# Performance work log

Hardware: AMD Instinct MI355X
Metric: run time of the kernel (lower is better)

The kernel has to match this reference:

```python
import jax, jax.numpy as jnp
import numpy as np

B = 16384      # batch
FEAT = 4096    # features
D = 64         # nearest_root_factors(4096) -> (64, 64)
BN_EPS = 1e-3


def setup_inputs() -> dict:
    key = jax.random.key(0)
    ks = jax.random.split(key, 9)
    stdv1 = 1.0 / np.sqrt(D)   # layer1: zero_initialization=False path
    stdv2 = 0.001              # layer2: zero_initialization=True path

    def u(k, shape, s):
        return jax.random.uniform(k, shape, minval=-s, maxval=s, dtype=jnp.float32)

    return {
        "inputs": jax.random.normal(ks[0], (B, FEAT), dtype=jnp.float32),
        "bn0_gamma": jnp.ones((FEAT,), jnp.float32),
        "bn0_beta": jnp.zeros((FEAT,), jnp.float32),
        "bn1_gamma": jnp.ones((FEAT,), jnp.float32),
        "bn1_beta": jnp.zeros((FEAT,), jnp.float32),
        # Kronecker layer 1 (left: weights (o2=input_dim1, o1=out_dim1); right: (d,d))
        "k1_lw": u(ks[1], (D, D), stdv1),
        "k1_lb": u(ks[2], (D, D), stdv1),
        "k1_rw": u(ks[3], (D, D), stdv1),
        "k1_rb": u(ks[4], (D, D), stdv1),
        # Kronecker layer 2 (zero-initialized)
        "k2_lw": u(ks[5], (D, D), stdv2),
        "k2_lb": u(ks[6], (D, D), stdv2),
        "k2_rw": u(ks[7], (D, D), stdv2),
        "k2_rb": u(ks[8], (D, D), stdv2),
    }


def _batch_norm(x, gamma, beta):
    # training-mode BN: biased batch statistics over the batch dim, eps=1e-3
    m = jnp.mean(x, axis=0)
    v = jnp.var(x, axis=0)
    return (x - m) * jax.lax.rsqrt(v + BN_EPS) * gamma + beta


def _kron_block(t, lw, lb, rw, rb):
    # KDLeftLayer: permute(matmul(permute(x,[0,2,1]), W),[0,2,1]) + b
    #   out[b,o,j] = sum_k x[b,k,j] * W[k,o]
    t = jnp.einsum("bkj,ko->boj", t, lw) + lb
    # KDRightLayer: x @ W + b
    t = jnp.matmul(t, rw) + rb
    return t


def reference(inputs, bn0_gamma, bn0_beta, bn1_gamma, bn1_beta,
              k1_lw, k1_lb, k1_rw, k1_rb, k2_lw, k2_lb, k2_rw, k2_rb):
    t = jax.nn.relu(_batch_norm(inputs, bn0_gamma, bn0_beta))
    t = t.reshape(-1, D, D)
    t = _kron_block(t, k1_lw, k1_lb, k1_rw, k1_rb).reshape(-1, FEAT)
    t = jax.nn.relu(_batch_norm(t, bn1_gamma, bn1_beta))
    # dropout p=0.0 -> identity
    t = t.reshape(-1, D, D)
    t = _kron_block(t, k2_lw, k2_lb, k2_rw, k2_rb).reshape(-1, FEAT)
    return inputs + t
```

## Files before the change

kernel.cpp:

```cpp
#include <hip/hip_runtime.h>

#define NROWS 16384
#define NFEAT 4096

typedef __attribute__((ext_vector_type(8))) short          bfrag8;
typedef __attribute__((ext_vector_type(4))) float          fvec4;
typedef __attribute__((ext_vector_type(2))) float          fvec2;
typedef __attribute__((ext_vector_type(4))) unsigned short usvec4;
typedef __attribute__((ext_vector_type(8))) unsigned short usvec8;
typedef __attribute__((ext_vector_type(2))) unsigned int   uvec2;

#define WS_P0   ((size_t)0)
#define WS_P1   ((size_t)16 << 20)
#define WS_SC0  ((size_t)48 << 20)
#define WS_SH0  (WS_SC0 + 16384)
#define WS_SC1  (WS_SC0 + 32768)
#define WS_SH1  (WS_SC0 + 49152)
#define WS_C1   (WS_SC0 + 65536)
#define WS_C2   (WS_SC0 + 81920)
#define WS_T1   ((size_t)64 << 20)
#define WS_XB   ((size_t)192 << 20)

__device__ __forceinline__ unsigned short f2bf_bits(float f) {
  unsigned u = __builtin_bit_cast(unsigned, f);
  u += 0x7FFFu + ((u >> 16) & 1u);
  return (unsigned short)(u >> 16);
}
__device__ __forceinline__ float bf2f(unsigned short b) {
  return __builtin_bit_cast(float, ((unsigned)b) << 16);
}
__device__ __forceinline__ usvec4 pack4(fvec4 a) {
  usvec4 p;
#pragma unroll
  for (int e = 0; e < 4; ++e) p[e] = f2bf_bits(a[e]);
  return p;
}
__device__ __forceinline__ fvec4 unpack4(usvec4 p) {
  return fvec4{bf2f(p[0]), bf2f(p[1]), bf2f(p[2]), bf2f(p[3])};
}

__global__ __launch_bounds__(256) void k_bn0part(const float* __restrict__ x,
                                                 unsigned short* __restrict__ p0,
                                                 unsigned short* __restrict__ xb) {
  const int t = threadIdx.x, p = blockIdx.x;
  fvec4 s[4], sq[4];
#pragma unroll
  for (int q = 0; q < 4; ++q) { s[q] = fvec4{0.f,0.f,0.f,0.f}; sq[q] = s[q]; }
  for (int r = p * 16; r < p * 16 + 16; ++r) {
    const fvec4* row = (const fvec4*)(x + (size_t)r * NFEAT);
    usvec4* xrow = (usvec4*)(xb + (size_t)r * NFEAT);
#pragma unroll
    for (int q = 0; q < 4; ++q) {
      fvec4 v = row[t + 256 * q];
      s[q] += v; sq[q] += v * v;
      xrow[t + 256 * q] = pack4(v);
    }
  }
#pragma unroll
  for (int q = 0; q < 4; ++q) {
    int f0 = (t + 256 * q) * 4;
    *(usvec4*)(p0 + (size_t)p * 8192 + f0)        = pack4(s[q]);
    *(usvec4*)(p0 + (size_t)p * 8192 + 4096 + f0) = pack4(sq[q]);
  }
}

__device__ __forceinline__ void red_body(fvec4 (*red)[16][2],
                                         const unsigned short* __restrict__ parts,
                                         int nsets,
                                         const float* __restrict__ g,
                                         const float* __restrict__ bta,
                                         float* __restrict__ sc_out,
                                         float* __restrict__ sh_out, int j) {
  const int t = threadIdx.x;
  const int fc = t & 15, c = t >> 4;
  const int v = j * 64 + fc * 4;
  fvec4 s = fvec4{0.f,0.f,0.f,0.f}, q = s;
  for (int i = c; i < nsets; i += 16) {
    s += unpack4(*(const usvec4*)(parts + (size_t)i * 8192 + v));
    q += unpack4(*(const usvec4*)(parts + (size_t)i * 8192 + 4096 + v));
  }
  red[c][fc][0] = s; red[c][fc][1] = q;
  __syncthreads();
  if (c == 0) {
    fvec4 S = red[0][fc][0], Q = red[0][fc][1];
#pragma unroll
    for (int k = 1; k < 16; ++k) { S += red[k][fc][0]; Q += red[k][fc][1]; }
    fvec4 SC, SH;
    const float inv = 1.0f / NROWS;
#pragma unroll
    for (int e = 0; e < 4; ++e) {
      float mean = S[e] * inv;
      float var  = Q[e] * inv - mean * mean;
      float scv  = g[v + e] * rsqrtf(var + 1e-3f);
      SC[e] = scv; SH[e] = bta[v + e] - mean * scv;
    }
    *(fvec4*)(sc_out + v) = SC;
    *(fvec4*)(sh_out + v) = SH;
  }
}

__global__ __launch_bounds__(256) void k_prep0(const unsigned short* __restrict__ p0,
                                               const float* __restrict__ g0,
                                               const float* __restrict__ b0,
                                               float* __restrict__ sc0,
                                               float* __restrict__ sh0,
                                               const float* __restrict__ lb1,
                                               const float* __restrict__ rw1,
                                               const float* __restrict__ rb1,
                                               const float* __restrict__ lb2,
                                               const float* __restrict__ rw2,
                                               const float* __restrict__ rb2,
                                               float* __restrict__ c1,
                                               float* __restrict__ c2) {
  __shared__ fvec4 red[16][16][2];
  if (blockIdx.x < 64) {
    red_body(red, p0, 1024, g0, b0, sc0, sh0, blockIdx.x);
  } else {
    const int bb   = blockIdx.x - 64;
    const int idx  = (bb & 15) * 256 + threadIdx.x;
    const int part = bb >> 4;
    const float* lb = part ? lb2 : lb1;
    const float* rw = part ? rw2 : rw1;
    const float* rb = part ? rb2 : rb1;
    int r = idx >> 6, o = idx & 63;
    float acc = rb[o * 64 + r];
    for (int j = 0; j < 64; ++j) acc += lb[o * 64 + j] * rw[j * 64 + r];
    (part ? c2 : c1)[o * 64 + r] = acc;
  }
}

__global__ __launch_bounds__(256) void k_red1(const unsigned short* __restrict__ p1,
                                              const float* __restrict__ g1,
                                              const float* __restrict__ b1,
                                              float* __restrict__ sc1,
                                              float* __restrict__ sh1) {
  __shared__ fvec4 red[16][16][2];
  red_body(red, p1, 2048, g1, b1, sc1, sh1, blockIdx.x);
}

template <int LAYER, int RPBN>
__global__ __launch_bounds__(256) void k_kron(const unsigned short* __restrict__ xb,
                                              const float* __restrict__ lw,
                                              const float* __restrict__ rw,
                                              const float* __restrict__ scv,
                                              const float* __restrict__ shv,
                                              const float* __restrict__ cn,
                                              unsigned char* __restrict__ t1q,
                                              float* __restrict__ outf,
                                              unsigned short* __restrict__ p1) {
  __shared__ unsigned short vt[2][64 * 64];
  const int tid = threadIdx.x, bid = blockIdx.x;
  const int w = tid >> 6, l = tid & 63, m = l & 15, g = l >> 4;
  const int r0 = bid * RPBN;

  bfrag8 frw[4][2];
#pragma unroll
  for (int rt = 0; rt < 4; ++rt)
#pragma unroll
    for (int ks = 0; ks < 2; ++ks)
#pragma unroll
      for (int i = 0; i < 8; ++i)
        frw[rt][ks][i] = (short)f2bf_bits(rw[(ks * 32 + g * 8 + i) * 64 + rt * 16 + m]);

  bfrag8 flw[2];
#pragma unroll
  for (int ks = 0; ks < 2; ++ks)
#pragma unroll
    for (int i = 0; i < 8; ++i)
      flw[ks][i] = (short)f2bf_bits(lw[(ks * 32 + g * 8 + i) * 64 + w * 16 + m]);

  fvec4 cb[4];
#pragma unroll
  for (int rt = 0; rt < 4; ++rt)
    cb[rt] = *(const fvec4*)(cn + (w * 16 + m) * 64 + rt * 16 + g * 4);

  float sc[2][8], sh[2][8];
#pragma unroll
  for (int ks = 0; ks < 2; ++ks) {
    int f = (w * 16 + m) * 64 + ks * 32 + g * 8;
    fvec4 a0 = *(const fvec4*)(scv + f), a1 = *(const fvec4*)(scv + f + 4);
    fvec4 h0 = *(const fvec4*)(shv + f), h1 = *(const fvec4*)(shv + f + 4);
#pragma unroll
    for (int e = 0; e < 4; ++e) {
      sc[ks][e] = a0[e]; sc[ks][4 + e] = a1[e];
      sh[ks][e] = h0[e]; sh[ks][4 + e] = h1[e];
    }
  }

  fvec4 s1[4], q1[4];
#pragma unroll
  for (int rt = 0; rt < 4; ++rt) { s1[rt] = fvec4{0.f,0.f,0.f,0.f}; q1[rt] = s1[rt]; }

  usvec8 pfa[2][2];
  uvec2  pfq[2][2];
  usvec4 pfr[2][4];

  if constexpr (LAYER == 1) {
    const usvec8* pt0 = (const usvec8*)(xb + (size_t)r0 * NFEAT);
    const usvec8* pt1 = (const usvec8*)(xb + (size_t)(r0 + 1) * NFEAT);
    pfa[0][0] = pt0[(w * 16 + m) * 8 + g];
    pfa[0][1] = pt0[(w * 16 + m) * 8 + 4 + g];
    pfa[1][0] = pt1[(w * 16 + m) * 8 + g];
    pfa[1][1] = pt1[(w * 16 + m) * 8 + 4 + g];
  } else {
    const uvec2* pq0 = (const uvec2*)(t1q + (size_t)r0 * NFEAT);
    const uvec2* pq1 = (const uvec2*)(t1q + (size_t)(r0 + 1) * NFEAT);
    pfq[0][0] = pq0[(w * 16 + m) * 8 + g];
    pfq[0][1] = pq0[(w * 16 + m) * 8 + 4 + g];
    pfq[1][0] = pq1[(w * 16 + m) * 8 + g];
    pfq[1][1] = pq1[(w * 16 + m) * 8 + 4 + g];
#pragma unroll
    for (int rt = 0; rt < 4; ++rt) {
      int off = (w * 16 + m) * 64 + rt * 16 + g * 4;
      pfr[0][rt] = *(const usvec4*)(xb + (size_t)r0 * NFEAT + off);
      pfr[1][rt] = *(const usvec4*)(xb + (size_t)(r0 + 1) * NFEAT + off);
    }
  }

#pragma unroll
  for (int rr = 0; rr < RPBN; ++rr) {
    const int b = r0 + rr;
    const int cur = rr & 1;

    bfrag8 fa[2];
    if constexpr (LAYER == 1) {
#pragma unroll
      for (int ks = 0; ks < 2; ++ks) {
        usvec8 tv = pfa[cur][ks];
#pragma unroll
        for (int i = 0; i < 8; ++i) {
          float y = fmaxf(bf2f(tv[i]) * sc[ks][i] + sh[ks][i], 0.f);
          fa[ks][i] = (short)f2bf_bits(y);
        }
      }
    } else {
#pragma unroll
      for (int ks = 0; ks < 2; ++ks) {
        uvec2 tv = pfq[cur][ks];
        fvec2 d0 = __builtin_amdgcn_cvt_pk_f32_fp8((int)tv[0], false);
        fvec2 d1 = __builtin_amdgcn_cvt_pk_f32_fp8((int)tv[0], true);
        fvec2 d2 = __builtin_amdgcn_cvt_pk_f32_fp8((int)tv[1], false);
        fvec2 d3 = __builtin_amdgcn_cvt_pk_f32_fp8((int)tv[1], true);
        float xv[8] = {d0[0], d0[1], d1[0], d1[1], d2[0], d2[1], d3[0], d3[1]};
#pragma unroll
        for (int i = 0; i < 8; ++i) {
          float y = fmaxf(xv[i] * sc[ks][i] + sh[ks][i], 0.f);
          fa[ks][i] = (short)f2bf_bits(y);
        }
      }
    }

    if (rr + 2 < RPBN) {
      if constexpr (LAYER == 1) {
        const usvec8* pt = (const usvec8*)(xb + (size_t)(b + 2) * NFEAT);
        pfa[cur][0] = pt[(w * 16 + m) * 8 + g];
        pfa[cur][1] = pt[(w * 16 + m) * 8 + 4 + g];
      } else {
        const uvec2* pq = (const uvec2*)(t1q + (size_t)(b + 2) * NFEAT);
        pfq[cur][0] = pq[(w * 16 + m) * 8 + g];
        pfq[cur][1] = pq[(w * 16 + m) * 8 + 4 + g];
      }
    }

#pragma unroll
    for (int rt = 0; rt < 4; ++rt) {
      fvec4 va = fvec4{0.f,0.f,0.f,0.f};
      va = __builtin_amdgcn_mfma_f32_16x16x32_bf16(fa[0], frw[rt][0], va, 0, 0, 0);
      va = __builtin_amdgcn_mfma_f32_16x16x32_bf16(fa[1], frw[rt][1], va, 0, 0, 0);
      int ridx = rt * 16 + m;
      int chunk = 2 * w + (g >> 1);
      int byte = ridx * 128 + ((chunk ^ (ridx & 7)) << 4) + ((g & 1) * 8);
      *(usvec4*)((char*)(&vt[cur][0]) + byte) = pack4(va);
    }

    __builtin_amdgcn_sched_barrier(0);
    asm volatile("s_waitcnt lgkmcnt(0)");
    __builtin_amdgcn_s_barrier();
    __builtin_amdgcn_sched_barrier(0);

    fvec4 za[4];
#pragma unroll
    for (int rt = 0; rt < 4; ++rt) za[rt] = fvec4{0.f,0.f,0.f,0.f};
#pragma unroll
    for (int ks = 0; ks < 2; ++ks) {
#pragma unroll
      for (int rt = 0; rt < 4; ++rt) {
        int ridx = rt * 16 + m;
        int byte = ridx * 128 + (((ks * 4 + g) ^ (ridx & 7)) << 4);
        bfrag8 av = *(const bfrag8*)((const char*)(&vt[cur][0]) + byte);
        za[rt] = __builtin_amdgcn_mfma_f32_16x16x32_bf16(av, flw[ks], za[rt], 0, 0, 0);
      }
    }

    if constexpr (LAYER == 1) {
#pragma unroll
      for (int rt = 0; rt < 4; ++rt) {
        fvec4 z = za[rt] + cb[rt];
        s1[rt] += z; q1[rt] += z * z;
        int pq = __builtin_amdgcn_cvt_pk_fp8_f32(z[0], z[1], 0, false);
        pq     = __builtin_amdgcn_cvt_pk_fp8_f32(z[2], z[3], pq, true);
        *(unsigned*)(t1q + (size_t)b * NFEAT +
                     (w * 16 + m) * 64 + rt * 16 + g * 4) = (unsigned)pq;
      }
    } else {
      fvec4* pout = (fvec4*)(outf + (size_t)b * NFEAT);
#pragma unroll
      for (int rt = 0; rt < 4; ++rt) {
        int fi = ((w * 16 + m) * 64 + rt * 16 + g * 4) >> 2;
        pout[fi] = unpack4(pfr[cur][rt]) + za[rt] + cb[rt];
      }
      if (rr + 2 < RPBN) {
#pragma unroll
        for (int rt = 0; rt < 4; ++rt) {
          int off = (w * 16 + m) * 64 + rt * 16 + g * 4;
          pfr[cur][rt] = *(const usvec4*)(xb + (size_t)(b + 2) * NFEAT + off);
        }
      }
    }
  }

  if constexpr (LAYER == 1) {
#pragma unroll
    for (int rt = 0; rt < 4; ++rt) {
      int vf = (w * 16 + m) * 64 + rt * 16 + g * 4;
      *(usvec4*)(p1 + (size_t)bid * 8192 + vf)        = pack4(s1[rt]);
      *(usvec4*)(p1 + (size_t)bid * 8192 + 4096 + vf) = pack4(q1[rt]);
    }
  }
}

extern "C" void kernel_launch(void* const* d_in, const int* in_sizes, int n_in,
                              void* d_out, int out_size, void* d_ws, size_t ws_size,
                              hipStream_t stream) {
  (void)in_sizes; (void)n_in; (void)out_size; (void)ws_size;
  const float* x    = (const float*)d_in[0];
  const float* g0   = (const float*)d_in[1];
  const float* b0   = (const float*)d_in[2];
  const float* g1   = (const float*)d_in[3];
  const float* b1   = (const float*)d_in[4];
  const float* k1lw = (const float*)d_in[5];
  const float* k1lb = (const float*)d_in[6];
  const float* k1rw = (const float*)d_in[7];
  const float* k1rb = (const float*)d_in[8];
  const float* k2lw = (const float*)d_in[9];
  const float* k2lb = (const float*)d_in[10];
  const float* k2rw = (const float*)d_in[11];
  const float* k2rb = (const float*)d_in[12];
  char* ws = (char*)d_ws;

  unsigned short* p0  = (unsigned short*)(ws + WS_P0);
  unsigned short* p1  = (unsigned short*)(ws + WS_P1);
  unsigned char*  t1q = (unsigned char*)(ws + WS_T1);
  unsigned short* xb  = (unsigned short*)(ws + WS_XB);
  float* sc0 = (float*)(ws + WS_SC0);
  float* sh0 = (float*)(ws + WS_SH0);
  float* sc1 = (float*)(ws + WS_SC1);
  float* sh1 = (float*)(ws + WS_SH1);
  float* c1  = (float*)(ws + WS_C1);
  float* c2  = (float*)(ws + WS_C2);

  k_bn0part<<<1024, 256, 0, stream>>>(x, p0, xb);
  k_prep0<<<96, 256, 0, stream>>>(p0, g0, b0, sc0, sh0,
                                  k1lb, k1rw, k1rb, k2lb, k2rw, k2rb, c1, c2);
  k_kron<1, 8><<<NROWS / 8, 256, 0, stream>>>(xb, k1lw, k1rw, sc0, sh0, c1,
                                              t1q, nullptr, p1);
  k_red1<<<64, 256, 0, stream>>>(p1, g1, b1, sc1, sh1);
  k_kron<2, 8><<<NROWS / 8, 256, 0, stream>>>(xb, k2lw, k2rw, sc1, sh1, c2,
                                              t1q, (float*)d_out, nullptr);
}
```

Baseline: 348.8 us.

## Give each wavefront whole rows in kron kernels and split out BN1 statistics

Restructures the Kronecker kernels so each wavefront processes an entire 64x64 row by itself, using a private LDS tile. This removes the per-row block-wide barrier, and scale/shift and bias constants are staged in LDS as packed bf16. The BN1 sum and sum-of-squares accumulation moves out of layer 1 into a new pass that reads the fp8 intermediate. That pass costs an extra read of the intermediate and computes statistics from the quantized values rather than fp32, which could change accuracy.

```diff
diff --git a/kernel.cpp b/kernel.cpp
--- a/kernel.cpp
+++ b/kernel.cpp
@@ -9,6 +9,7 @@
 typedef __attribute__((ext_vector_type(4))) unsigned short usvec4;
 typedef __attribute__((ext_vector_type(8))) unsigned short usvec8;
 typedef __attribute__((ext_vector_type(2))) unsigned int   uvec2;
+typedef __attribute__((ext_vector_type(4))) unsigned int   uvec4;
 
 #define WS_P0   ((size_t)0)
 #define WS_P1   ((size_t)16 << 20)
@@ -38,6 +39,8 @@
 __device__ __forceinline__ fvec4 unpack4(usvec4 p) {
   return fvec4{bf2f(p[0]), bf2f(p[1]), bf2f(p[2]), bf2f(p[3])};
 }
+__device__ __forceinline__ int swz64(int i) { return i ^ (((i >> 6) & 7) << 2); }
+__device__ __forceinline__ int swz32(int i) { return i ^ (((i >> 5) & 7) << 2); }
 
 __global__ __launch_bounds__(256) void k_bn0part(const float* __restrict__ x,
                                                  unsigned short* __restrict__ p0,
@@ -129,29 +132,75 @@
   }
 }
 
+__global__ __launch_bounds__(256) void k_bn1stat(const unsigned char* __restrict__ t1q,
+                                                 unsigned short* __restrict__ p1) {
+  const int t = threadIdx.x, p = blockIdx.x;
+  float s[16], q[16];
+#pragma unroll
+  for (int i = 0; i < 16; ++i) { s[i] = 0.f; q[i] = 0.f; }
+  for (int r = p * 16; r < p * 16 + 16; ++r) {
+    uvec4 v = *(const uvec4*)(t1q + (size_t)r * NFEAT + t * 16);
+#pragma unroll
+    for (int d = 0; d < 4; ++d) {
+      fvec2 lo = __builtin_amdgcn_cvt_pk_f32_fp8((int)v[d], false);
+      fvec2 hi = __builtin_amdgcn_cvt_pk_f32_fp8((int)v[d], true);
+      float e0 = lo[0], e1 = lo[1], e2 = hi[0], e3 = hi[1];
+      s[d*4+0] += e0; q[d*4+0] += e0*e0;
+      s[d*4+1] += e1; q[d*4+1] += e1*e1;
+      s[d*4+2] += e2; q[d*4+2] += e2*e2;
+      s[d*4+3] += e3; q[d*4+3] += e3*e3;
+    }
+  }
+#pragma unroll
+  for (int b4 = 0; b4 < 4; ++b4) {
+    fvec4 sv{s[b4*4], s[b4*4+1], s[b4*4+2], s[b4*4+3]};
+    fvec4 qv{q[b4*4], q[b4*4+1], q[b4*4+2], q[b4*4+3]};
+    *(usvec4*)(p1 + (size_t)p * 8192 + t * 16 + b4 * 4)        = pack4(sv);
+    *(usvec4*)(p1 + (size_t)p * 8192 + 4096 + t * 16 + b4 * 4) = pack4(qv);
+  }
+}
+
 __global__ __launch_bounds__(256) void k_red1(const unsigned short* __restrict__ p1,
                                               const float* __restrict__ g1,
                                               const float* __restrict__ b1,
                                               float* __restrict__ sc1,
                                               float* __restrict__ sh1) {
   __shared__ fvec4 red[16][16][2];
-  red_body(red, p1, 2048, g1, b1, sc1, sh1, blockIdx.x);
-}
-
-template <int LAYER, int RPBN>
-__global__ __launch_bounds__(256) void k_kron(const unsigned short* __restrict__ xb,
-                                              const float* __restrict__ lw,
-                                              const float* __restrict__ rw,
-                                              const float* __restrict__ scv,
-                                              const float* __restrict__ shv,
-                                              const float* __restrict__ cn,
-                                              unsigned char* __restrict__ t1q,
-                                              float* __restrict__ outf,
-                                              unsigned short* __restrict__ p1) {
-  __shared__ unsigned short vt[2][64 * 64];
+  red_body(red, p1, 1024, g1, b1, sc1, sh1, blockIdx.x);
+}
+
+template <int LAYER>
+__global__ __launch_bounds__(256, 2) void k_kron(const unsigned short* __restrict__ xb,
+                                                 const unsigned char* __restrict__ t1r,
+                                                 const float* __restrict__ lw,
+                                                 const float* __restrict__ rw,
+                                                 const float* __restrict__ scv,
+                                                 const float* __restrict__ shv,
+                                                 const float* __restrict__ cn,
+                                                 unsigned char* __restrict__ t1w,
+                                                 float* __restrict__ outf) {
+  __shared__ __align__(16) unsigned short vt[4][4096];
+  __shared__ __align__(16) unsigned scsh[4096];
+  __shared__ __align__(16) unsigned cbl[2048];
   const int tid = threadIdx.x, bid = blockIdx.x;
   const int w = tid >> 6, l = tid & 63, m = l & 15, g = l >> 4;
-  const int r0 = bid * RPBN;
+  unsigned short* vtw = &vt[w][0];
+
+#pragma unroll
+  for (int c = 0; c < 16; ++c) {
+    int f = tid * 16 + c;
+    scsh[swz64(f)] = (unsigned)f2bf_bits(scv[f]) | ((unsigned)f2bf_bits(shv[f]) << 16);
+  }
+#pragma unroll
+  for (int c = 0; c < 8; ++c) {
+    int d = tid * 8 + c;
+    int o = d >> 5, pr = (d & 31) * 2;
+    cbl[swz32(d)] = (unsigned)f2bf_bits(cn[o * 64 + pr]) |
+                    ((unsigned)f2bf_bits(cn[o * 64 + pr + 1]) << 16);
+  }
+#pragma unroll
+  for (int c = 0; c < 8; ++c)
+    *(uvec4*)((char*)vtw + l * 128 + c * 16) = uvec4{0u, 0u, 0u, 0u};
 
   bfrag8 frw[4][2];
 #pragma unroll
@@ -162,170 +211,154 @@
       for (int i = 0; i < 8; ++i)
         frw[rt][ks][i] = (short)f2bf_bits(rw[(ks * 32 + g * 8 + i) * 64 + rt * 16 + m]);
 
-  bfrag8 flw[2];
-#pragma unroll
-  for (int ks = 0; ks < 2; ++ks)
-#pragma unroll
-    for (int i = 0; i < 8; ++i)
-      flw[ks][i] = (short)f2bf_bits(lw[(ks * 32 + g * 8 + i) * 64 + w * 16 + m]);
-
-  fvec4 cb[4];
-#pragma unroll
-  for (int rt = 0; rt < 4; ++rt)
-    cb[rt] = *(const fvec4*)(cn + (w * 16 + m) * 64 + rt * 16 + g * 4);
-
-  float sc[2][8], sh[2][8];
-#pragma unroll
-  for (int ks = 0; ks < 2; ++ks) {
-    int f = (w * 16 + m) * 64 + ks * 32 + g * 8;
-    fvec4 a0 = *(const fvec4*)(scv + f), a1 = *(const fvec4*)(scv + f + 4);
-    fvec4 h0 = *(const fvec4*)(shv + f), h1 = *(const fvec4*)(shv + f + 4);
-#pragma unroll
-    for (int e = 0; e < 4; ++e) {
-      sc[ks][e] = a0[e]; sc[ks][4 + e] = a1[e];
-      sh[ks][e] = h0[e]; sh[ks][4 + e] = h1[e];
-    }
-  }
-
-  fvec4 s1[4], q1[4];
-#pragma unroll
-  for (int rt = 0; rt < 4; ++rt) { s1[rt] = fvec4{0.f,0.f,0.f,0.f}; q1[rt] = s1[rt]; }
-
-  usvec8 pfa[2][2];
-  uvec2  pfq[2][2];
-  usvec4 pfr[2][4];
+  bfrag8 flw[4][2];
+#pragma unroll
+  for (int ot = 0; ot < 4; ++ot)
+#pragma unroll
+    for (int ks = 0; ks < 2; ++ks)
+#pragma unroll
+      for (int i = 0; i < 8; ++i)
+        flw[ot][ks][i] = (short)f2bf_bits(lw[(ks * 32 + g * 8 + i) * 64 + ot * 16 + m]);
+
+  __syncthreads();
+
+  const int r0w = bid * 32 + w * 8;
+
+  usvec8 sA0[8], sA1[8];
+  uvec2  sQ0[8], sQ1[8];
 
   if constexpr (LAYER == 1) {
-    const usvec8* pt0 = (const usvec8*)(xb + (size_t)r0 * NFEAT);
-    const usvec8* pt1 = (const usvec8*)(xb + (size_t)(r0 + 1) * NFEAT);
-    pfa[0][0] = pt0[(w * 16 + m) * 8 + g];
-    pfa[0][1] = pt0[(w * 16 + m) * 8 + 4 + g];
-    pfa[1][0] = pt1[(w * 16 + m) * 8 + g];
-    pfa[1][1] = pt1[(w * 16 + m) * 8 + 4 + g];
+    const usvec8* p = (const usvec8*)(xb + (size_t)r0w * NFEAT);
+#pragma unroll
+    for (int kt = 0; kt < 4; ++kt)
+#pragma unroll
+      for (int ks = 0; ks < 2; ++ks)
+        sA0[kt * 2 + ks] = p[(kt * 16 + m) * 8 + ks * 4 + g];
   } else {
-    const uvec2* pq0 = (const uvec2*)(t1q + (size_t)r0 * NFEAT);
-    const uvec2* pq1 = (const uvec2*)(t1q + (size_t)(r0 + 1) * NFEAT);
-    pfq[0][0] = pq0[(w * 16 + m) * 8 + g];
-    pfq[0][1] = pq0[(w * 16 + m) * 8 + 4 + g];
-    pfq[1][0] = pq1[(w * 16 + m) * 8 + g];
-    pfq[1][1] = pq1[(w * 16 + m) * 8 + 4 + g];
-#pragma unroll
-    for (int rt = 0; rt < 4; ++rt) {
-      int off = (w * 16 + m) * 64 + rt * 16 + g * 4;
-      pfr[0][rt] = *(const usvec4*)(xb + (size_t)r0 * NFEAT + off);
-      pfr[1][rt] = *(const usvec4*)(xb + (size_t)(r0 + 1) * NFEAT + off);
-    }
-  }
-
-#pragma unroll
-  for (int rr = 0; rr < RPBN; ++rr) {
-    const int b = r0 + rr;
-    const int cur = rr & 1;
-
-    bfrag8 fa[2];
-    if constexpr (LAYER == 1) {
+    const uvec2* p = (const uvec2*)(t1r + (size_t)r0w * NFEAT);
+#pragma unroll
+    for (int kt = 0; kt < 4; ++kt)
+#pragma unroll
+      for (int ks = 0; ks < 2; ++ks)
+        sQ0[kt * 2 + ks] = p[(kt * 16 + m) * 8 + ks * 4 + g];
+  }
+
+  auto row_body = [&](int rrow, usvec8 (&curA)[8], usvec8 (&nxtA)[8],
+                      uvec2 (&curQ)[8], uvec2 (&nxtQ)[8], bool pf) {
+    if (pf) {
+      if constexpr (LAYER == 1) {
+        const usvec8* p = (const usvec8*)(xb + (size_t)(rrow + 1) * NFEAT);
+#pragma unroll
+        for (int kt = 0; kt < 4; ++kt)
+#pragma unroll
+          for (int ks = 0; ks < 2; ++ks)
+            nxtA[kt * 2 + ks] = p[(kt * 16 + m) * 8 + ks * 4 + g];
+      } else {
+        const uvec2* p = (const uvec2*)(t1r + (size_t)(rrow + 1) * NFEAT);
+#pragma unroll
+        for (int kt = 0; kt < 4; ++kt)
+#pragma unroll
+          for (int ks = 0; ks < 2; ++ks)
+            nxtQ[kt * 2 + ks] = p[(kt * 16 + m) * 8 + ks * 4 + g];
+      }
+    }
+    usvec4 res[16];
+    if constexpr (LAYER == 2) {
+#pragma unroll
+      for (int ot = 0; ot < 4; ++ot)
+#pragma unroll
+        for (int rt2 = 0; rt2 < 4; ++rt2)
+          res[ot * 4 + rt2] = *(const usvec4*)(xb + (size_t)rrow * NFEAT +
+                                               (ot * 16 + m) * 64 + rt2 * 16 + g * 4);
+    }
+
+#pragma unroll
+    for (int kt = 0; kt < 4; ++kt) {
+      bfrag8 fa[2];
 #pragma unroll
       for (int ks = 0; ks < 2; ++ks) {
-        usvec8 tv = pfa[cur][ks];
+        int f0 = (kt * 16 + m) * 64 + ks * 32 + g * 8;
+        uvec4 c0  = *(const uvec4*)&scsh[swz64(f0)];
+        uvec4 c1v = *(const uvec4*)&scsh[swz64(f0 + 4)];
+        float xs[8];
+        if constexpr (LAYER == 1) {
+          usvec8 tv = curA[kt * 2 + ks];
+#pragma unroll
+          for (int i = 0; i < 8; ++i) xs[i] = bf2f(tv[i]);
+        } else {
+          uvec2 tv = curQ[kt * 2 + ks];
+          fvec2 d0 = __builtin_amdgcn_cvt_pk_f32_fp8((int)tv[0], false);
+          fvec2 d1 = __builtin_amdgcn_cvt_pk_f32_fp8((int)tv[0], true);
+          fvec2 d2 = __builtin_amdgcn_cvt_pk_f32_fp8((int)tv[1], false);
+          fvec2 d3 = __builtin_amdgcn_cvt_pk_f32_fp8((int)tv[1], true);
+          xs[0]=d0[0]; xs[1]=d0[1]; xs[2]=d1[0]; xs[3]=d1[1];
+          xs[4]=d2[0]; xs[5]=d2[1]; xs[6]=d3[0]; xs[7]=d3[1];
+        }
+        usvec8 u;
 #pragma unroll
         for (int i = 0; i < 8; ++i) {
-          float y = fmaxf(bf2f(tv[i]) * sc[ks][i] + sh[ks][i], 0.f);
-          fa[ks][i] = (short)f2bf_bits(y);
+          unsigned dw = (i < 4) ? c0[i] : c1v[i - 4];
+          float scf = __builtin_bit_cast(float, dw << 16);
+          float shf = __builtin_bit_cast(float, dw & 0xffff0000u);
+          u[i] = f2bf_bits(fmaxf(fmaf(xs[i], scf, shf), 0.f));
+        }
+        fa[ks] = __builtin_bit_cast(bfrag8, u);
+      }
+#pragma unroll
+      for (int rt = 0; rt < 4; ++rt) {
+        fvec4 va = fvec4{0.f, 0.f, 0.f, 0.f};
+        va = __builtin_amdgcn_mfma_f32_16x16x32_bf16(fa[0], frw[rt][0], va, 0, 0, 0);
+        va = __builtin_amdgcn_mfma_f32_16x16x32_bf16(fa[1], frw[rt][1], va, 0, 0, 0);
+        int ridx = rt * 16 + m;
+        int chunk = 2 * kt + (g >> 1);
+        int byte = ridx * 128 + ((chunk ^ (ridx & 7)) << 4) + (g & 1) * 8;
+        *(usvec4*)((char*)vtw + byte) = pack4(va);
+      }
+    }
+
+    __builtin_amdgcn_sched_barrier(0);
+    asm volatile("s_waitcnt lgkmcnt(0)");
+    __builtin_amdgcn_sched_barrier(0);
+
+#pragma unroll
+    for (int rt2 = 0; rt2 < 4; ++rt2) {
+      int ridx = rt2 * 16 + m;
+      bfrag8 a0 = *(const bfrag8*)((const char*)vtw +
+                    ridx * 128 + (((0 + g) ^ (ridx & 7)) << 4));
+      bfrag8 a1 = *(const bfrag8*)((const char*)vtw +
+                    ridx * 128 + (((4 + g) ^ (ridx & 7)) << 4));
+      fvec4 acc[4];
+#pragma unroll
+      for (int ot = 0; ot < 4; ++ot) {
+        acc[ot] = fvec4{0.f, 0.f, 0.f, 0.f};
+        acc[ot] = __builtin_amdgcn_mfma_f32_16x16x32_bf16(a0, flw[ot][0], acc[ot], 0, 0, 0);
+        acc[ot] = __builtin_amdgcn_mfma_f32_16x16x32_bf16(a1, flw[ot][1], acc[ot], 0, 0, 0);
+      }
+#pragma unroll
+      for (int ot = 0; ot < 4; ++ot) {
+        int dcb = (ot * 16 + m) * 32 + rt2 * 8 + 2 * g;
+        uvec2 cv = *(const uvec2*)&cbl[swz32(dcb)];
+        fvec4 cb4{__builtin_bit_cast(float, cv[0] << 16),
+                  __builtin_bit_cast(float, cv[0] & 0xffff0000u),
+                  __builtin_bit_cast(float, cv[1] << 16),
+                  __builtin_bit_cast(float, cv[1] & 0xffff0000u)};
+        fvec4 z = acc[ot] + cb4;
+        int foff = (ot * 16 + m) * 64 + rt2 * 16 + g * 4;
+        if constexpr (LAYER == 1) {
+          int pq = __builtin_amdgcn_cvt_pk_fp8_f32(z[0], z[1], 0, false);
+          pq     = __builtin_amdgcn_cvt_pk_fp8_f32(z[2], z[3], pq, true);
+          *(unsigned*)(t1w + (size_t)rrow * NFEAT + foff) = (unsigned)pq;
+        } else {
+          *(fvec4*)(outf + (size_t)rrow * NFEAT + foff) =
+              unpack4(res[ot * 4 + rt2]) + z;
         }
       }
-    } else {
-#pragma unroll
-      for (int ks = 0; ks < 2; ++ks) {
-        uvec2 tv = pfq[cur][ks];
-        fvec2 d0 = __builtin_amdgcn_cvt_pk_f32_fp8((int)tv[0], false);
-        fvec2 d1 = __builtin_amdgcn_cvt_pk_f32_fp8((int)tv[0], true);
-        fvec2 d2 = __builtin_amdgcn_cvt_pk_f32_fp8((int)tv[1], false);
-        fvec2 d3 = __builtin_amdgcn_cvt_pk_f32_fp8((int)tv[1], true);
-        float xv[8] = {d0[0], d0[1], d1[0], d1[1], d2[0], d2[1], d3[0], d3[1]};
-#pragma unroll
-        for (int i = 0; i < 8; ++i) {
-          float y = fmaxf(xv[i] * sc[ks][i] + sh[ks][i], 0.f);
-          fa[ks][i] = (short)f2bf_bits(y);
-        }
-      }
-    }
-
-    if (rr + 2 < RPBN) {
-      if constexpr (LAYER == 1) {
-        const usvec8* pt = (const usvec8*)(xb + (size_t)(b + 2) * NFEAT);
-        pfa[cur][0] = pt[(w * 16 + m) * 8 + g];
-        pfa[cur][1] = pt[(w * 16 + m) * 8 + 4 + g];
-      } else {
-        const uvec2* pq = (const uvec2*)(t1q + (size_t)(b + 2) * NFEAT);
-        pfq[cur][0] = pq[(w * 16 + m) * 8 + g];
-        pfq[cur][1] = pq[(w * 16 + m) * 8 + 4 + g];
-      }
-    }
-
-#pragma unroll
-    for (int rt = 0; rt < 4; ++rt) {
-      fvec4 va = fvec4{0.f,0.f,0.f,0.f};
-      va = __builtin_amdgcn_mfma_f32_16x16x32_bf16(fa[0], frw[rt][0], va, 0, 0, 0);
-      va = __builtin_amdgcn_mfma_f32_16x16x32_bf16(fa[1], frw[rt][1], va, 0, 0, 0);
-      int ridx = rt * 16 + m;
-      int chunk = 2 * w + (g >> 1);
-      int byte = ridx * 128 + ((chunk ^ (ridx & 7)) << 4) + ((g & 1) * 8);
-      *(usvec4*)((char*)(&vt[cur][0]) + byte) = pack4(va);
-    }
-
-    __builtin_amdgcn_sched_barrier(0);
-    asm volatile("s_waitcnt lgkmcnt(0)");
-    __builtin_amdgcn_s_barrier();
-    __builtin_amdgcn_sched_barrier(0);
-
-    fvec4 za[4];
-#pragma unroll
-    for (int rt = 0; rt < 4; ++rt) za[rt] = fvec4{0.f,0.f,0.f,0.f};
-#pragma unroll
-    for (int ks = 0; ks < 2; ++ks) {
-#pragma unroll
-      for (int rt = 0; rt < 4; ++rt) {
-        int ridx = rt * 16 + m;
-        int byte = ridx * 128 + (((ks * 4 + g) ^ (ridx & 7)) << 4);
-        bfrag8 av = *(const bfrag8*)((const char*)(&vt[cur][0]) + byte);
-        za[rt] = __builtin_amdgcn_mfma_f32_16x16x32_bf16(av, flw[ks], za[rt], 0, 0, 0);
-      }
-    }
-
-    if constexpr (LAYER == 1) {
-#pragma unroll
-      for (int rt = 0; rt < 4; ++rt) {
-        fvec4 z = za[rt] + cb[rt];
-        s1[rt] += z; q1[rt] += z * z;
-        int pq = __builtin_amdgcn_cvt_pk_fp8_f32(z[0], z[1], 0, false);
-        pq     = __builtin_amdgcn_cvt_pk_fp8_f32(z[2], z[3], pq, true);
-        *(unsigned*)(t1q + (size_t)b * NFEAT +
-                     (w * 16 + m) * 64 + rt * 16 + g * 4) = (unsigned)pq;
-      }
-    } else {
-      fvec4* pout = (fvec4*)(outf + (size_t)b * NFEAT);
-#pragma unroll
-      for (int rt = 0; rt < 4; ++rt) {
-        int fi = ((w * 16 + m) * 64 + rt * 16 + g * 4) >> 2;
-        pout[fi] = unpack4(pfr[cur][rt]) + za[rt] + cb[rt];
-      }
-      if (rr + 2 < RPBN) {
-#pragma unroll
-        for (int rt = 0; rt < 4; ++rt) {
-          int off = (w * 16 + m) * 64 + rt * 16 + g * 4;
-          pfr[cur][rt] = *(const usvec4*)(xb + (size_t)(b + 2) * NFEAT + off);
-        }
-      }
-    }
-  }
-
-  if constexpr (LAYER == 1) {
-#pragma unroll
-    for (int rt = 0; rt < 4; ++rt) {
-      int vf = (w * 16 + m) * 64 + rt * 16 + g * 4;
-      *(usvec4*)(p1 + (size_t)bid * 8192 + vf)        = pack4(s1[rt]);
-      *(usvec4*)(p1 + (size_t)bid * 8192 + 4096 + vf) = pack4(q1[rt]);
-    }
+    }
+  };
+
+  for (int rp = 0; rp < 4; ++rp) {
+    row_body(r0w + 2 * rp,     sA0, sA1, sQ0, sQ1, true);
+    row_body(r0w + 2 * rp + 1, sA1, sA0, sQ1, sQ0, rp < 3);
   }
 }
 
@@ -362,9 +395,10 @@
   k_bn0part<<<1024, 256, 0, stream>>>(x, p0, xb);
   k_prep0<<<96, 256, 0, stream>>>(p0, g0, b0, sc0, sh0,
                                   k1lb, k1rw, k1rb, k2lb, k2rw, k2rb, c1, c2);
-  k_kron<1, 8><<<NROWS / 8, 256, 0, stream>>>(xb, k1lw, k1rw, sc0, sh0, c1,
-                                              t1q, nullptr, p1);
+  k_kron<1><<<512, 256, 0, stream>>>(xb, nullptr, k1lw, k1rw, sc0, sh0, c1,
+                                     t1q, nullptr);
+  k_bn1stat<<<1024, 256, 0, stream>>>(t1q, p1);
   k_red1<<<64, 256, 0, stream>>>(p1, g1, b1, sc1, sh1);
-  k_kron<2, 8><<<NROWS / 8, 256, 0, stream>>>(xb, k2lw, k2rw, sc1, sh1, c2,
-                                              t1q, (float*)d_out, nullptr);
-}
+  k_kron<2><<<512, 256, 0, stream>>>(xb, t1q, k2lw, k2rw, sc1, sh1, c2,
+                                     t1q, (float*)d_out);
+}
```

After: 326.1 us. 1.07x faster.
